# Kernel optimization log

Hardware: AMD Instinct MI355X
Metric: run time of the kernel (lower is better)

The kernel has to match this reference:

```python
import jax, jax.numpy as jnp
import numpy as np

N, E, B = 20000, 160000, 1024
MDIM, EDIM, H, L, PROP = 64, 16, 128, 4, 1000


def _lin(key, fan_in, fan_out, scale=None):
    s = scale if scale is not None else 1.0 / np.sqrt(fan_in)
    return (jax.random.normal(key, (fan_in, fan_out), jnp.float32) * s)


def setup_inputs() -> dict:
    key = jax.random.key(0)
    ks = iter(jax.random.split(key, 64))
    d = {}
    d["x"] = jax.random.normal(next(ks), (N, MDIM), jnp.float32)
    d["pos"] = jax.random.normal(next(ks), (N, 3), jnp.float32)
    d["edge_attr"] = jax.random.normal(next(ks), (E, EDIM), jnp.float32)
    d["edge_index"] = jax.random.randint(next(ks), (2, E), 0, N)
    d["batch"] = jnp.sort(jax.random.randint(next(ks), (N,), 0, B))
    # EGNN embeddings
    d["emb_in_w"] = _lin(next(ks), MDIM, H); d["emb_in_b"] = jnp.zeros((H,), jnp.float32)
    d["emb_out_w"] = _lin(next(ks), H, H); d["emb_out_b"] = jnp.zeros((H,), jnp.float32)
    # per-layer E_GCL params, stacked over layers
    ein = 2 * H + 1 + EDIM  # [h_row, h_col, radial, edge_attr]
    d["edge_w1"] = jnp.stack([_lin(next(ks), ein, H) for _ in range(L)]); d["edge_b1"] = jnp.zeros((L, H), jnp.float32)
    d["edge_w2"] = jnp.stack([_lin(next(ks), H, H) for _ in range(L)]); d["edge_b2"] = jnp.zeros((L, H), jnp.float32)
    d["node_w1"] = jnp.stack([_lin(next(ks), 2 * H, H) for _ in range(L)]); d["node_b1"] = jnp.zeros((L, H), jnp.float32)
    d["node_w2"] = jnp.stack([_lin(next(ks), H, H) for _ in range(L)]); d["node_b2"] = jnp.zeros((L, H), jnp.float32)
    d["coord_w1"] = jnp.stack([_lin(next(ks), H, H) for _ in range(L)]); d["coord_b1"] = jnp.zeros((L, H), jnp.float32)
    d["coord_w2"] = jnp.stack([_lin(next(ks), H, 1, scale=0.001) for _ in range(L)])  # xavier gain=0.001, no bias
    # end_layers: 2 ResBlocks (Dropout->Linear->SiLU->Linear) + head
    d["res_w1"] = jnp.stack([_lin(next(ks), H, H) for _ in range(2)]); d["res_b1"] = jnp.zeros((2, H), jnp.float32)
    d["res_w2"] = jnp.stack([_lin(next(ks), H, H) for _ in range(2)]); d["res_b2"] = jnp.zeros((2, H), jnp.float32)
    d["head_w"] = _lin(next(ks), H, PROP); d["head_b"] = jnp.zeros((PROP,), jnp.float32)
    return d


def _egnn_forward(x, pos, edge_attr, edge_index, batch,
                  emb_in_w, emb_in_b, emb_out_w, emb_out_b,
                  edge_w1, edge_b1, edge_w2, edge_b2,
                  node_w1, node_b1, node_w2, node_b2,
                  coord_w1, coord_b1, coord_w2,
                  res_w1, res_b1, res_w2, res_b2, head_w, head_b):
    silu = jax.nn.silu
    row, col = edge_index[0], edge_index[1]
    h = x @ emb_in_w + emb_in_b                                   # [N, H]
    # edge in-degree counts for coords_agg='mean' (clamped to >=1)
    cnt = jax.ops.segment_sum(jnp.ones((E, 1), h.dtype), row, num_segments=N)
    cnt = jnp.maximum(cnt, 1.0)
    for l in range(L):
        coord_diff = pos[row] - pos[col]                          # [E, 3]
        radial = jnp.sum(coord_diff * coord_diff, axis=-1, keepdims=True)  # [E, 1]
        # edge model
        e_in = jnp.concatenate([h[row], h[col], radial, edge_attr], axis=-1)
        m = silu(silu(e_in @ edge_w1[l] + edge_b1[l]) @ edge_w2[l] + edge_b2[l])  # [E, H]
        # coord model (coords_agg='mean')
        trans = coord_diff * (silu(m @ coord_w1[l] + coord_b1[l]) @ coord_w2[l])  # [E, 3]
        pos = pos + jax.ops.segment_sum(trans, row, num_segments=N) / cnt
        # node model (residual=True)
        agg = jax.ops.segment_sum(m, row, num_segments=N)         # [N, H]
        n_in = jnp.concatenate([h, agg], axis=-1)
        h = h + (silu(n_in @ node_w1[l] + node_b1[l]) @ node_w2[l] + node_b2[l])
    h = h @ emb_out_w + emb_out_b
    g = jax.ops.segment_max(h, batch, num_segments=B)             # [B, H]
    for r in range(2):
        g = g + (silu(g @ res_w1[r] + res_b1[r]) @ res_w2[r] + res_b2[r])
    return g @ head_w + head_b                                    # [B, PROP]


def reference(x, pos, edge_attr, edge_index, batch,
              emb_in_w, emb_in_b, emb_out_w, emb_out_b,
              edge_w1, edge_b1, edge_w2, edge_b2,
              node_w1, node_b1, node_w2, node_b2,
              coord_w1, coord_b1, coord_w2,
              res_w1, res_b1, res_w2, res_b2, head_w, head_b):
    return _egnn_forward(x, pos, edge_attr, edge_index, batch,
                         emb_in_w, emb_in_b, emb_out_w, emb_out_b,
                         edge_w1, edge_b1, edge_w2, edge_b2,
                         node_w1, node_b1, node_w2, node_b2,
                         coord_w1, coord_b1, coord_w2,
                         res_w1, res_b1, res_w2, res_b2, head_w, head_b)
```

## Files before the change

### kernel.cpp

```cpp
#include <hip/hip_runtime.h>
#include <hip/hip_bf16.h>

#define HD 128
#define PROP 1000
#define NPB  8

typedef float f32x4 __attribute__((ext_vector_type(4)));
typedef short s16x8 __attribute__((ext_vector_type(8)));

__device__ __forceinline__ float silu_f(float v) { return v / (1.0f + __expf(-v)); }

__device__ __forceinline__ unsigned short f2bf(float f) {
    union { __hip_bfloat16 h; unsigned short u; } v;
    v.h = __float2bfloat16(f);
    return v.u;
}
__device__ __forceinline__ unsigned pk2(float a, float b) {
    union { __hip_bfloat162 h; unsigned u; } v;
    v.h = __float22bfloat162_rn(make_float2(a, b));
    return v.u;
}
__device__ __forceinline__ float bf2f_lo(unsigned u) { return __uint_as_float(u << 16); }
__device__ __forceinline__ float bf2f_hi(unsigned u) { return __uint_as_float(u & 0xffff0000u); }
__device__ __forceinline__ float4 ld4(const float* p) { return *(const float4*)p; }
__device__ __forceinline__ unsigned enc_max(float f) {
    unsigned u = __float_as_uint(f);
    return (u & 0x80000000u) ? ~u : (u | 0x80000000u);
}


__global__ void counti_kernel(const int* __restrict__ ei, int* __restrict__ cnt, int E) {
    int e = blockIdx.x * 256 + threadIdx.x;
    if (e < E) atomicAdd(&cnt[ei[e]], 1);
}

__global__ __launch_bounds__(1024) void scan_blk(
    const int* __restrict__ cnt, int* __restrict__ excl, int* __restrict__ bsum, int N)
{
    __shared__ int wsum[16], wexc[17];
    const int t = threadIdx.x, lane = t & 63, wid = t >> 6;
    const int gid = blockIdx.x * 1024 + t;
    int v = (gid < N) ? cnt[gid] : 0;
    int incl = v;
    #pragma unroll
    for (int d = 1; d < 64; d <<= 1) {
        int x = __shfl_up(incl, d, 64);
        if (lane >= d) incl += x;
    }
    if (lane == 63) wsum[wid] = incl;
    __syncthreads();
    if (t == 0) {
        int a = 0;
        #pragma unroll
        for (int w2 = 0; w2 < 16; ++w2) { wexc[w2] = a; a += wsum[w2]; }
        wexc[16] = a;
    }
    __syncthreads();
    if (gid < N) excl[gid] = wexc[wid] + incl - v;
    if (t == 0) bsum[blockIdx.x] = wexc[16];
}
__global__ __launch_bounds__(64) void scan_top(int* __restrict__ bsum, int nb) {
    const int lane = threadIdx.x;
    int v = (lane < nb) ? bsum[lane] : 0;
    int incl = v;
    #pragma unroll
    for (int d = 1; d < 64; d <<= 1) {
        int x = __shfl_up(incl, d, 64);
        if (lane >= d) incl += x;
    }
    if (lane < nb) bsum[lane] = incl - v;
}
__global__ void scan_add(const int* __restrict__ excl, const int* __restrict__ bsum,
                         int* __restrict__ rp, int* __restrict__ wp, int N, int E) {
    int gid = blockIdx.x * 256 + threadIdx.x;
    if (gid < N) {
        int r = excl[gid] + bsum[gid >> 10];
        rp[gid] = r; wp[gid] = r;
    }
    if (gid == 0) rp[N] = E;
}

__global__ void scatter_kernel(const int* __restrict__ ei, int* __restrict__ wp,
                               int* __restrict__ perm, int* __restrict__ rows_s,
                               int* __restrict__ cols_s, int E) {
    int e = blockIdx.x * 256 + threadIdx.x;
    if (e < E) {
        int r = ei[e];
        int p = atomicAdd(&wp[r], 1);
        perm[p] = e;
        rows_s[p] = r;
        cols_s[p] = ei[E + e];
    }
}

__global__ void eattr_perm_kernel(const float* __restrict__ eattr, const int* __restrict__ perm,
                                  unsigned short* __restrict__ eperm, int E) {
    int i = blockIdx.x * 256 + threadIdx.x;
    if (i >= E) return;
    const float* src = eattr + (size_t)perm[i] * 16;
    float4 a = ld4(src), b = ld4(src + 4), c = ld4(src + 8), d = ld4(src + 12);
    unsigned short* dst = eperm + (size_t)i * 16;
    *(uint4*)dst       = make_uint4(pk2(a.x, a.y), pk2(a.z, a.w), pk2(b.x, b.y), pk2(b.z, b.w));
    *(uint4*)(dst + 8) = make_uint4(pk2(c.x, c.y), pk2(c.z, c.w), pk2(d.x, d.y), pk2(d.z, d.w));
}

__global__ void prep_all(
    const float* __restrict__ ew1, const float* __restrict__ ew2, const float* __restrict__ cw1,
    const float* __restrict__ nw1, const float* __restrict__ nw2,
    const float* __restrict__ emb_in_w, const float* __restrict__ emb_out_w,
    unsigned short* __restrict__ w1nc, unsigned short* __restrict__ wattr,
    unsigned short* __restrict__ wt2, unsigned short* __restrict__ cwt1,
    unsigned short* __restrict__ nw1t, unsigned short* __restrict__ nw2t,
    unsigned short* __restrict__ wembt, unsigned short* __restrict__ wot,
    unsigned* __restrict__ g_enc, int ng)
{
    int idx = blockIdx.x * 256 + threadIdx.x;
    if (idx < 131072) {
        int k = idx & 127, o2 = (idx >> 7) & 255, l = idx >> 15;
        w1nc[idx] = f2bf(ew1[((size_t)l * 273 + k + ((o2 >> 7) << 7)) * 128 + (o2 & 127)]);
        return;
    }
    idx -= 131072;
    if (idx < 16384) {
        int k = idx & 31, o = (idx >> 5) & 127, l = idx >> 12;
        int ksrc = (k < 16) ? (257 + k) : (k == 16 ? 256 : -1);
        float v = (ksrc >= 0) ? ew1[((size_t)l * 273 + ksrc) * 128 + o] : 0.0f;
        wattr[idx] = f2bf(v);
        return;
    }
    idx -= 16384;
    if (idx < 65536) {
        int k = idx & 127, o = (idx >> 7) & 127, l = idx >> 14;
        int ks = ((k >> 2) & 7) * 16 + ((k >> 5) << 2) + (k & 3);
        wt2[idx] = f2bf(ew2[((size_t)l * 128 + ks) * 128 + o]);
        return;
    }
    idx -= 65536;
    if (idx < 65536) {
        int k = idx & 127, o = (idx >> 7) & 127, l = idx >> 14;
        cwt1[idx] = f2bf(cw1[((size_t)l * 128 + k) * 128 + o]);
        return;
    }
    idx -= 65536;
    if (idx < 131072) {
        int k = idx % 256, o = (idx / 256) & 127, l = idx / (256 * 128);
        nw1t[idx] = f2bf(nw1[((size_t)l * 256 + k) * 128 + o]);
        return;
    }
    idx -= 131072;
    if (idx < 65536) {
        int k = idx & 127, o = (idx >> 7) & 127, l = idx >> 14;
        nw2t[idx] = f2bf(nw2[((size_t)l * 128 + k) * 128 + o]);
        return;
    }
    idx -= 65536;
    if (idx < 8192) {
        int k = idx & 63, o = idx >> 6;
        wembt[idx] = f2bf(emb_in_w[(size_t)k * 128 + o]);
        return;
    }
    idx -= 8192;
    if (idx < 16384) {
        int k = idx & 127, o = idx >> 7;
        wot[idx] = f2bf(emb_out_w[(size_t)k * 128 + o]);
        return;
    }
    idx -= 16384;
    if (idx < ng) g_enc[idx] = 0x007FFFFFu;
}

__global__ __launch_bounds__(128) void emb_pre_kernel(
    const float* __restrict__ x, const unsigned short* __restrict__ wembt,
    const float* __restrict__ bemb,
    const unsigned short* __restrict__ w1nc, const float* __restrict__ b1,
    float* __restrict__ h, unsigned short* __restrict__ apre, int N)
{
    __shared__ __align__(16) char s_xt[32 * 128];
    __shared__ __align__(16) char s_h[32 * 256];
    const int tid = threadIdx.x;
    const int lane = tid & 63, wid = tid >> 6;
    const int lr = lane & 15, kg = lane >> 4;
    const int n0 = blockIdx.x * 32 + wid * 16;
    {
        int n16 = lane >> 2, q = lane & 3;
        int nn = min(n0 + n16, N - 1);
        int sw2 = (n16 & 7) << 4;
        char* row = s_xt + (wid * 16 + n16) * 128;
        #pragma unroll
        for (int it = 0; it < 4; ++it) {
            float4 v = ld4(x + (size_t)nn * 64 + q * 16 + it * 4);
            *(uint2*)(row + ((q * 32 + it * 8) ^ sw2)) = make_uint2(pk2(v.x, v.y), pk2(v.z, v.w));
        }
    }
    const int nd = n0 + lr;
    const int sw = (lr & 7) << 4;
    f32x4 acc[8];
    #pragma unroll
    for (int mf = 0; mf < 8; ++mf) acc[mf] = (f32x4){0.f, 0.f, 0.f, 0.f};
    {
        const char* brow = s_xt + (wid * 16 + lr) * 128;
        for (int ks = 0; ks < 2; ++ks) {
            s16x8 b = *(const s16x8*)(brow + ((ks * 64 + kg * 16) ^ sw));
            #pragma unroll
            for (int mf = 0; mf < 8; ++mf) {
                s16x8 a = *(const s16x8*)(wembt + (size_t)(mf * 16 + lr) * 64 + ks * 32 + kg * 8);
                acc[mf] = __builtin_amdgcn_mfma_f32_16x16x32_bf16(a, b, acc[mf], 0, 0, 0);
            }
        }
    }
    char* hrow = s_h + (wid * 16 + lr) * 256;
    #pragma unroll
    for (int mf = 0; mf < 8; ++mf) {
        f32x4 bb = *(const f32x4*)(bemb + mf * 16 + kg * 4);
        float v0 = acc[mf][0] + bb[0];
        float v1 = acc[mf][1] + bb[1];
        float v2 = acc[mf][2] + bb[2];
        float v3 = acc[mf][3] + bb[3];
        if (nd < N) *(f32x4*)(h + (size_t)nd * HD + mf * 16 + kg * 4) = (f32x4){v0, v1, v2, v3};
        *(uint2*)(hrow + ((mf * 32 + kg * 8) ^ sw)) = make_uint2(pk2(v0, v1), pk2(v2, v3));
    }
    f32x4 acc2[16];
    #pragma unroll
    for (int mf = 0; mf < 16; ++mf) acc2[mf] = (f32x4){0.f, 0.f, 0.f, 0.f};
    for (int ks = 0; ks < 4; ++ks) {
        s16x8 b = *(const s16x8*)(hrow + ((ks * 64 + kg * 16) ^ sw));
        #pragma unroll
        for (int mf = 0; mf < 16; ++mf) {
            s16x8 a = *(const s16x8*)(w1nc + (size_t)(mf * 16 + lr) * 128 + ks * 32 + kg * 8);
            acc2[mf] = __builtin_amdgcn_mfma_f32_16x16x32_bf16(a, b, acc2[mf], 0, 0, 0);
        }
    }
    if (nd < N) {
        #pragma unroll
        for (int mf = 0; mf < 16; ++mf) {
            float b0 = 0.f, b1v = 0.f, b2v = 0.f, b3v = 0.f;
            if (mf < 8) {
                f32x4 bb = *(const f32x4*)(b1 + mf * 16 + kg * 4);
                b0 = bb[0]; b1v = bb[1]; b2v = bb[2]; b3v = bb[3];
            }
            int pos = ((mf >> 3) << 7) + kg * 32 + (mf & 7) * 4;
            *(uint2*)(apre + (size_t)nd * 256 + pos) =
                make_uint2(pk2(acc2[mf][0] + b0, acc2[mf][1] + b1v), pk2(acc2[mf][2] + b2v, acc2[mf][3] + b3v));
        }
    }
}

__global__ __launch_bounds__(64) void edge_compute_kernel(
    const float* __restrict__ pos, const unsigned short* __restrict__ apre,
    const unsigned short* __restrict__ eperm,
    const int* __restrict__ rows_s, const int* __restrict__ cols_s,
    const unsigned short* __restrict__ wattr,
    const unsigned short* __restrict__ wt2, const float* __restrict__ b2,
    const unsigned short* __restrict__ cwt1, const float* __restrict__ cb1,
    const float* __restrict__ cw2,
    unsigned short* __restrict__ medge, float* __restrict__ trans, int E)
{
    __shared__ __align__(16) char s_m[2][16 * 256];
    __shared__ __align__(16) char s_g[2][16 * 256];

    int wg = blockIdx.x;
    {
        int nper = gridDim.x >> 3;
        if ((gridDim.x & 7) == 0) wg = (wg & 7) * nper + (wg >> 3);
    }
    const int lane = threadIdx.x;
    const int lr = lane & 15, kg = lane >> 4;
    const int i0 = wg * 32;
    const int iA = i0 + lr, iB = i0 + 16 + lr;
    const bool vA = iA < E, vB = iB < E;
    const int icA = min(iA, E - 1), icB = min(iB, E - 1);
    const int rA = rows_s[icA], cA = cols_s[icA];
    const int rB = rows_s[icB], cB = cols_s[icB];

    {
        int e = lane >> 2, q = lane & 3;
        int sw2 = (e & 7) << 4;
        #pragma unroll
        for (int t = 0; t < 2; ++t) {
            int ce = cols_s[min(i0 + t * 16 + e, E - 1)];
            const char* src = (const char*)(apre + (size_t)ce * 256 + 128);
            char* dst = s_g[t] + e * 256;
            #pragma unroll
            for (int it = 0; it < 4; ++it) {
                uint4 v = *(const uint4*)(src + it * 64 + q * 16);
                *(uint4*)(dst + ((it * 64 + q * 16) ^ sw2)) = v;
            }
        }
    }

    float dxA = pos[rA*3+0] - pos[cA*3+0];
    float dyA = pos[rA*3+1] - pos[cA*3+1];
    float dzA = pos[rA*3+2] - pos[cA*3+2];
    float dxB = pos[rB*3+0] - pos[cB*3+0];
    float dyB = pos[rB*3+1] - pos[cB*3+1];
    float dzB = pos[rB*3+2] - pos[cB*3+2];
    float radA = dxA*dxA + dyA*dyA + dzA*dzA;
    float radB = dxB*dxB + dyB*dyB + dzB*dzB;

    union { s16x8 v; unsigned u[4]; } battrA, battrB;
    if (kg < 2) {
        battrA.v = *(const s16x8*)(eperm + (size_t)icA * 16 + kg * 8);
        battrB.v = *(const s16x8*)(eperm + (size_t)icB * 16 + kg * 8);
    } else {
        battrA.u[0] = (kg == 2) ? pk2(radA, 0.f) : 0u;
        battrA.u[1] = 0u; battrA.u[2] = 0u; battrA.u[3] = 0u;
        battrB.u[0] = (kg == 2) ? pk2(radB, 0.f) : 0u;
        battrB.u[1] = 0u; battrB.u[2] = 0u; battrB.u[3] = 0u;
    }

    char* mrowA = s_m[0] + lr * 256;
    char* mrowB = s_m[1] + lr * 256;
    const int sw = (lr & 7) << 4;

    f32x4 aA[8], aB[8];
    #pragma unroll
    for (int mf = 0; mf < 8; ++mf) { aA[mf] = (f32x4){0,0,0,0}; aB[mf] = (f32x4){0,0,0,0}; }

    #pragma unroll
    for (int mf = 0; mf < 8; ++mf) {
        s16x8 a = *(const s16x8*)(wattr + (size_t)(mf * 16 + lr) * 32 + kg * 8);
        aA[mf] = __builtin_amdgcn_mfma_f32_16x16x32_bf16(a, battrA.v, aA[mf], 0, 0, 0);
        aB[mf] = __builtin_amdgcn_mfma_f32_16x16x32_bf16(a, battrB.v, aB[mf], 0, 0, 0);
    }
    #pragma unroll
    for (int t = 0; t < 2; ++t) {
        const int r = t ? rB : rA;
        f32x4* acc = t ? aB : aA;
        char* mrow = t ? mrowB : mrowA;
        uint4 rgq[4], cgq[4];
        {
            const unsigned short* rb = apre + (size_t)r * 256 + kg * 32;
            const char* g = s_g[t] + lr * 256;
            #pragma unroll
            for (int q = 0; q < 4; ++q) {
                rgq[q] = *(const uint4*)(rb + q * 8);
                cgq[q] = *(const uint4*)(g + ((kg * 64 + q * 16) ^ sw));
            }
        }
        #pragma unroll
        for (int mf = 0; mf < 8; ++mf) {
            unsigned rlo = ((const unsigned*)&rgq[mf >> 1])[(mf & 1) * 2];
            unsigned rhi = ((const unsigned*)&rgq[mf >> 1])[(mf & 1) * 2 + 1];
            unsigned clo = ((const unsigned*)&cgq[mf >> 1])[(mf & 1) * 2];
            unsigned chi = ((const unsigned*)&cgq[mf >> 1])[(mf & 1) * 2 + 1];
            float v0 = silu_f(acc[mf][0] + bf2f_lo(rlo) + bf2f_lo(clo));
            float v1 = silu_f(acc[mf][1] + bf2f_hi(rlo) + bf2f_hi(clo));
            float v2 = silu_f(acc[mf][2] + bf2f_lo(rhi) + bf2f_lo(chi));
            float v3 = silu_f(acc[mf][3] + bf2f_hi(rhi) + bf2f_hi(chi));
            *(uint2*)(mrow + ((kg * 64 + mf * 8) ^ sw)) = make_uint2(pk2(v0, v1), pk2(v2, v3));
        }
    }

    #pragma unroll
    for (int mf = 0; mf < 8; ++mf) { aA[mf] = (f32x4){0,0,0,0}; aB[mf] = (f32x4){0,0,0,0}; }
    for (int ks = 0; ks < 4; ++ks) {
        s16x8 bA = *(const s16x8*)(mrowA + ((ks * 64 + kg * 16) ^ sw));
        s16x8 bB = *(const s16x8*)(mrowB + ((ks * 64 + kg * 16) ^ sw));
        #pragma unroll
        for (int mf = 0; mf < 8; ++mf) {
            s16x8 a = *(const s16x8*)(wt2 + (size_t)(mf * 16 + lr) * 128 + ks * 32 + kg * 8);
            aA[mf] = __builtin_amdgcn_mfma_f32_16x16x32_bf16(a, bA, aA[mf], 0, 0, 0);
            aB[mf] = __builtin_amdgcn_mfma_f32_16x16x32_bf16(a, bB, aB[mf], 0, 0, 0);
        }
    }
    #pragma unroll
    for (int t = 0; t < 2; ++t) {
        f32x4* acc = t ? aB : aA;
        char* mrow = t ? mrowB : mrowA;
        #pragma unroll
        for (int mf = 0; mf < 8; ++mf) {
            f32x4 bb = *(const f32x4*)(b2 + mf * 16 + kg * 4);
            float v0 = silu_f(acc[mf][0] + bb[0]);
            float v1 = silu_f(acc[mf][1] + bb[1]);
            float v2 = silu_f(acc[mf][2] + bb[2]);
            float v3 = silu_f(acc[mf][3] + bb[3]);
            *(uint2*)(mrow + ((mf * 32 + kg * 8) ^ sw)) = make_uint2(pk2(v0, v1), pk2(v2, v3));
        }
    }

    #pragma unroll
    for (int mf = 0; mf < 8; ++mf) { aA[mf] = (f32x4){0,0,0,0}; aB[mf] = (f32x4){0,0,0,0}; }
    for (int ks = 0; ks < 4; ++ks) {
        s16x8 bA = *(const s16x8*)(mrowA + ((ks * 64 + kg * 16) ^ sw));
        s16x8 bB = *(const s16x8*)(mrowB + ((ks * 64 + kg * 16) ^ sw));
        #pragma unroll
        for (int mf = 0; mf < 8; ++mf) {
            s16x8 a = *(const s16x8*)(cwt1 + (size_t)(mf * 16 + lr) * 128 + ks * 32 + kg * 8);
            aA[mf] = __builtin_amdgcn_mfma_f32_16x16x32_bf16(a, bA, aA[mf], 0, 0, 0);
            aB[mf] = __builtin_amdgcn_mfma_f32_16x16x32_bf16(a, bB, aB[mf], 0, 0, 0);
        }
    }

    {
        int e = lane >> 2, q = lane & 3;
        int sw2 = (e & 7) << 4;
        #pragma unroll
        for (int t = 0; t < 2; ++t) {
            int ie = i0 + t * 16 + e;
            if (ie < E) {
                const char* src = s_m[t] + e * 256;
                char* dst = (char*)(medge + (size_t)ie * HD);
                #pragma unroll
                for (int it = 0; it < 4; ++it) {
                    uint4 v = *(const uint4*)(src + ((it * 64 + q * 16) ^ sw2));
                    *(uint4*)(dst + it * 64 + q * 16) = v;
                }
            }
        }
    }

    #pragma unroll
    for (int t = 0; t < 2; ++t) {
        f32x4* acc = t ? aB : aA;
        float part = 0.f;
        #pragma unroll
        for (int mf = 0; mf < 8; ++mf) {
            f32x4 bb = *(const f32x4*)(cb1 + mf * 16 + kg * 4);
            f32x4 cw = *(const f32x4*)(cw2 + mf * 16 + kg * 4);
            part += silu_f(acc[mf][0] + bb[0]) * cw[0];
            part += silu_f(acc[mf][1] + bb[1]) * cw[1];
            part += silu_f(acc[mf][2] + bb[2]) * cw[2];
            part += silu_f(acc[mf][3] + bb[3]) * cw[3];
        }
        part += __shfl_xor(part, 16, 64);
        part += __shfl_xor(part, 32, 64);
        if (kg == 0) {
            int ie = i0 + t * 16 + lr;
            if (ie < E) {
                float dx = t ? dxB : dxA, dy = t ? dyB : dyA, dz = t ? dzB : dzA;
                *(float4*)(trans + (size_t)ie * 4) = make_float4(dx * part, dy * part, dz * part, 0.f);
            }
        }
    }
}

__global__ __launch_bounds__(64) void node_fused_kernel(
    float* __restrict__ h, const unsigned short* __restrict__ medge,
    const float* __restrict__ trans, const int* __restrict__ rp,
    float* __restrict__ pos,
    const unsigned short* __restrict__ nw1t, const float* __restrict__ nb1,
    const unsigned short* __restrict__ nw2t, const float* __restrict__ nb2,
    const unsigned short* __restrict__ w1nc_next, const float* __restrict__ b1_next,
    unsigned short* __restrict__ apre, int N, int has_next)
{
    __shared__ __align__(16) char s_x[16 * 512];
    const int lane = threadIdx.x;
    const int lr = lane & 15, kg = lane >> 4;
    const int n0 = blockIdx.x * 16;
    {
        int n16 = lane >> 2, q = lane & 3;
        int nn = min(n0 + n16, N - 1);
        int sw2 = (n16 & 7) << 4;
        char* row = s_x + n16 * 512;
        #pragma unroll
        for (int it = 0; it < 8; ++it) {
            int c2 = q * 32 + it * 4;
            float4 v = ld4(h + (size_t)nn * HD + c2);
            *(uint2*)(row + ((c2 * 2) ^ sw2)) = make_uint2(pk2(v.x, v.y), pk2(v.z, v.w));
        }
        const int s = rp[nn], e2 = rp[nn + 1];
        float a[32];
        #pragma unroll
        for (int t = 0; t < 32; ++t) a[t] = 0.f;
        for (int j = s; j < e2; ++j) {
            const unsigned short* mp = medge + (size_t)j * HD + q * 32;
            #pragma unroll
            for (int v4 = 0; v4 < 4; ++v4) {
                uint4 w = *(const uint4*)(mp + v4 * 8);
                a[v4*8+0] += bf2f_lo(w.x); a[v4*8+1] += bf2f_hi(w.x);
                a[v4*8+2] += bf2f_lo(w.y); a[v4*8+3] += bf2f_hi(w.y);
                a[v4*8+4] += bf2f_lo(w.z); a[v4*8+5] += bf2f_hi(w.z);
                a[v4*8+6] += bf2f_lo(w.w); a[v4*8+7] += bf2f_hi(w.w);
            }
        }
        #pragma unroll
        for (int it2 = 0; it2 < 4; ++it2) {
            uint4 w = make_uint4(pk2(a[it2*8+0], a[it2*8+1]), pk2(a[it2*8+2], a[it2*8+3]),
                                 pk2(a[it2*8+4], a[it2*8+5]), pk2(a[it2*8+6], a[it2*8+7]));
            *(uint4*)(row + ((256 + q * 64 + it2 * 16) ^ sw2)) = w;
        }
        if (q < 3 && n0 + n16 < N) {
            float pa = 0.f;
            for (int j = s; j < e2; ++j) pa += trans[(size_t)j * 4 + q];
            pos[(size_t)(n0 + n16) * 3 + q] += pa / fmaxf((float)(e2 - s), 1.0f);
        }
    }
    const int nd = n0 + lr;
    char* brow = s_x + lr * 512;
    const int sw = (lr & 7) << 4;
    f32x4 acc[8];
    #pragma unroll
    for (int mf = 0; mf < 8; ++mf) acc[mf] = (f32x4){0.f, 0.f, 0.f, 0.f};
    for (int ks = 0; ks < 8; ++ks) {
        s16x8 b = *(const s16x8*)(brow + ((ks * 64 + kg * 16) ^ sw));
        #pragma unroll
        for (int mf = 0; mf < 8; ++mf) {
            s16x8 a = *(const s16x8*)(nw1t + (size_t)(mf * 16 + lr) * 256 + ks * 32 + kg * 8);
            acc[mf] = __builtin_amdgcn_mfma_f32_16x16x32_bf16(a, b, acc[mf], 0, 0, 0);
        }
    }
    #pragma unroll
    for (int mf = 0; mf < 8; ++mf) {
        f32x4 bb = *(const f32x4*)(nb1 + mf * 16 + kg * 4);
        float v0 = silu_f(acc[mf][0] + bb[0]);
        float v1 = silu_f(acc[mf][1] + bb[1]);
        float v2 = silu_f(acc[mf][2] + bb[2]);
        float v3 = silu_f(acc[mf][3] + bb[3]);
        *(uint2*)(brow + ((mf * 32 + kg * 8) ^ sw)) = make_uint2(pk2(v0, v1), pk2(v2, v3));
    }
    #pragma unroll
    for (int mf = 0; mf < 8; ++mf) acc[mf] = (f32x4){0.f, 0.f, 0.f, 0.f};
    for (int ks = 0; ks < 4; ++ks) {
        s16x8 b = *(const s16x8*)(brow + ((ks * 64 + kg * 16) ^ sw));
        #pragma unroll
        for (int mf = 0; mf < 8; ++mf) {
            s16x8 a = *(const s16x8*)(nw2t + (size_t)(mf * 16 + lr) * 128 + ks * 32 + kg * 8);
            acc[mf] = __builtin_amdgcn_mfma_f32_16x16x32_bf16(a, b, acc[mf], 0, 0, 0);
        }
    }
    uint2 hpk[8];
    if (nd < N) {
        #pragma unroll
        for (int mf = 0; mf < 8; ++mf) {
            f32x4 bb = *(const f32x4*)(nb2 + mf * 16 + kg * 4);
            float* hp = h + (size_t)nd * HD + mf * 16 + kg * 4;
            f32x4 hv = *(const f32x4*)hp;
            hv[0] += acc[mf][0] + bb[0];
            hv[1] += acc[mf][1] + bb[1];
            hv[2] += acc[mf][2] + bb[2];
            hv[3] += acc[mf][3] + bb[3];
            *(f32x4*)hp = hv;
            hpk[mf] = make_uint2(pk2(hv[0], hv[1]), pk2(hv[2], hv[3]));
        }
    }
    if (!has_next) return;
    #pragma unroll
    for (int mf = 0; mf < 8; ++mf)
        *(uint2*)(brow + ((mf * 32 + kg * 8) ^ sw)) = hpk[mf];
    f32x4 acc2[16];
    #pragma unroll
    for (int mf = 0; mf < 16; ++mf) acc2[mf] = (f32x4){0.f, 0.f, 0.f, 0.f};
    for (int ks = 0; ks < 4; ++ks) {
        s16x8 b = *(const s16x8*)(brow + ((ks * 64 + kg * 16) ^ sw));
        #pragma unroll
        for (int mf = 0; mf < 16; ++mf) {
            s16x8 a = *(const s16x8*)(w1nc_next + (size_t)(mf * 16 + lr) * 128 + ks * 32 + kg * 8);
            acc2[mf] = __builtin_amdgcn_mfma_f32_16x16x32_bf16(a, b, acc2[mf], 0, 0, 0);
        }
    }
    if (nd < N) {
        #pragma unroll
        for (int mf = 0; mf < 16; ++mf) {
            float b0 = 0.f, b1v = 0.f, b2v = 0.f, b3v = 0.f;
            if (mf < 8) {
                f32x4 bb = *(const f32x4*)(b1_next + mf * 16 + kg * 4);
                b0 = bb[0]; b1v = bb[1]; b2v = bb[2]; b3v = bb[3];
            }
            int pos2 = ((mf >> 3) << 7) + kg * 32 + (mf & 7) * 4;
            *(uint2*)(apre + (size_t)nd * 256 + pos2) =
                make_uint2(pk2(acc2[mf][0] + b0, acc2[mf][1] + b1v), pk2(acc2[mf][2] + b2v, acc2[mf][3] + b3v));
        }
    }
}

__global__ __launch_bounds__(64) void embout_mfma_kernel(
    const float* __restrict__ h, const unsigned short* __restrict__ wot,
    const float* __restrict__ b, const int* __restrict__ batch,
    unsigned* __restrict__ g_enc, int N)
{
    __shared__ __align__(16) char s_h[16 * 256];
    __shared__ __align__(16) float s_out[16 * 128];
    const int lane = threadIdx.x;
    const int lr = lane & 15, kg = lane >> 4;
    const int n0 = blockIdx.x * 16;
    {
        int n16 = lane >> 2, q = lane & 3;
        int nn = min(n0 + n16, N - 1);
        int sw2 = (n16 & 7) << 4;
        char* row = s_h + n16 * 256;
        #pragma unroll
        for (int it = 0; it < 8; ++it) {
            int c2 = q * 32 + it * 4;
            float4 v = ld4(h + (size_t)nn * HD + c2);
            *(uint2*)(row + ((c2 * 2) ^ sw2)) = make_uint2(pk2(v.x, v.y), pk2(v.z, v.w));
        }
    }
    const char* brow = s_h + lr * 256;
    const int sw = (lr & 7) << 4;
    f32x4 acc[8];
    #pragma unroll
    for (int mf = 0; mf < 8; ++mf) acc[mf] = (f32x4){0.f, 0.f, 0.f, 0.f};
    for (int ks = 0; ks < 4; ++ks) {
        s16x8 bv = *(const s16x8*)(brow + ((ks * 64 + kg * 16) ^ sw));
        #pragma unroll
        for (int mf = 0; mf < 8; ++mf) {
            s16x8 a = *(const s16x8*)(wot + (size_t)(mf * 16 + lr) * 128 + ks * 32 + kg * 8);
            acc[mf] = __builtin_amdgcn_mfma_f32_16x16x32_bf16(a, bv, acc[mf], 0, 0, 0);
        }
    }
    #pragma unroll
    for (int mf = 0; mf < 8; ++mf) {
        f32x4 bb = *(const f32x4*)(b + mf * 16 + kg * 4);
        f32x4 v = { acc[mf][0] + bb[0], acc[mf][1] + bb[1], acc[mf][2] + bb[2], acc[mf][3] + bb[3] };
        *(f32x4*)(s_out + lr * 128 + mf * 16 + kg * 4) = v;
    }
    const int nmax = min(16, N - n0);
    float m0 = -3.4e38f, m1 = -3.4e38f;
    int cur = batch[n0];
    for (int e = 0; e < nmax; ++e) {
        int bi = batch[n0 + e];
        if (bi != cur) {
            atomicMax(&g_enc[(size_t)cur * HD + lane], enc_max(m0));
            atomicMax(&g_enc[(size_t)cur * HD + 64 + lane], enc_max(m1));
            m0 = -3.4e38f; m1 = -3.4e38f; cur = bi;
        }
        m0 = fmaxf(m0, s_out[e * 128 + lane]);
        m1 = fmaxf(m1, s_out[e * 128 + 64 + lane]);
    }
    atomicMax(&g_enc[(size_t)cur * HD + lane], enc_max(m0));
    atomicMax(&g_enc[(size_t)cur * HD + 64 + lane], enc_max(m1));
}

__global__ __launch_bounds__(128) void resblock_kernel(
    const unsigned* __restrict__ g_enc,
    const float* __restrict__ rw1, const float* __restrict__ rb1,
    const float* __restrict__ rw2, const float* __restrict__ rb2,
    float* __restrict__ g)
{
    __shared__ float s_g[HD];
    __shared__ float s_t[HD];
    const int b = blockIdx.x, j = threadIdx.x;
    unsigned u = g_enc[(size_t)b * HD + j];
    float v = (u & 0x80000000u) ? __uint_as_float(u & 0x7FFFFFFFu) : __uint_as_float(~u);
    s_g[j] = v;
    __syncthreads();
    for (int r = 0; r < 2; ++r) {
        float a1 = rb1[r * HD + j];
        for (int k = 0; k < HD; ++k) a1 += s_g[k] * rw1[(size_t)r * HD * HD + (size_t)k * HD + j];
        s_t[j] = silu_f(a1);
        __syncthreads();
        float a2 = rb2[r * HD + j];
        for (int k = 0; k < HD; ++k) a2 += s_t[k] * rw2[(size_t)r * HD * HD + (size_t)k * HD + j];
        __syncthreads();
        s_g[j] += a2;
        __syncthreads();
    }
    g[(size_t)b * HD + j] = s_g[j];
}

__global__ __launch_bounds__(256) void head_kernel(
    const float* __restrict__ g, const float* __restrict__ hw, const float* __restrict__ hb,
    float* __restrict__ out, int B)
{
    __shared__ __align__(16) float s_g[HD][8];
    const int b0 = blockIdx.y * 8;
    const int p = blockIdx.x * 256 + threadIdx.x;
    for (int t = threadIdx.x; t < 8 * HD; t += 256) {
        int b = t & 7, k = t >> 3;
        s_g[k][b] = g[(size_t)min(b0 + b, B - 1) * HD + k];
    }
    __syncthreads();
    if (p >= PROP) return;
    float hbp = hb[p];
    float acc[8];
    #pragma unroll
    for (int b = 0; b < 8; ++b) acc[b] = hbp;
    for (int k = 0; k < HD; ++k) {
        float w = hw[(size_t)k * PROP + p];
        float4 g0 = *(const float4*)&s_g[k][0];
        float4 g1 = *(const float4*)&s_g[k][4];
        acc[0] += g0.x * w; acc[1] += g0.y * w; acc[2] += g0.z * w; acc[3] += g0.w * w;
        acc[4] += g1.x * w; acc[5] += g1.y * w; acc[6] += g1.z * w; acc[7] += g1.w * w;
    }
    #pragma unroll
    for (int b = 0; b < 8; ++b)
        if (b0 + b < B) out[(size_t)(b0 + b) * PROP + p] = acc[b];
}

extern "C" void kernel_launch(void* const* d_in, const int* in_sizes, int n_in,
                              void* d_out, int out_size, void* d_ws, size_t ws_size,
                              hipStream_t stream)
{
    const float* x        = (const float*)d_in[0];
    const float* pos_in   = (const float*)d_in[1];
    const float* eattr    = (const float*)d_in[2];
    const int*   ei       = (const int*)d_in[3];
    const int*   batch    = (const int*)d_in[4];
    const float* emb_in_w = (const float*)d_in[5];
    const float* emb_in_b = (const float*)d_in[6];
    const float* emb_out_w= (const float*)d_in[7];
    const float* emb_out_b= (const float*)d_in[8];
    const float* ew1 = (const float*)d_in[9];
    const float* eb1 = (const float*)d_in[10];
    const float* ew2 = (const float*)d_in[11];
    const float* eb2 = (const float*)d_in[12];
    const float* nw1 = (const float*)d_in[13];
    const float* nb1 = (const float*)d_in[14];
    const float* nw2 = (const float*)d_in[15];
    const float* nb2 = (const float*)d_in[16];
    const float* cw1 = (const float*)d_in[17];
    const float* cb1 = (const float*)d_in[18];
    const float* cw2 = (const float*)d_in[19];
    const float* rw1 = (const float*)d_in[20];
    const float* rb1 = (const float*)d_in[21];
    const float* rw2 = (const float*)d_in[22];
    const float* rb2 = (const float*)d_in[23];
    const float* hw  = (const float*)d_in[24];
    const float* hb  = (const float*)d_in[25];
    float* out = (float*)d_out;
    (void)ws_size;

    const int N = in_sizes[0] / 64;
    const int E = in_sizes[2] / 16;
    const int B = out_size / PROP;

    float* wsf = (float*)d_ws;
    float* pos_cur = wsf;   wsf += (size_t)N * 3;
    float* h       = wsf;   wsf += (size_t)N * HD;
    float* g       = wsf;   wsf += (size_t)B * HD;
    float* trans   = wsf;   wsf += (size_t)E * 4;
    wsf += (4 - (((size_t)(wsf - (float*)d_ws)) & 3)) & 3;
    unsigned short* apre  = (unsigned short*)wsf;
    unsigned short* eperm = apre  + (size_t)N * 256;
    unsigned short* w1nc  = eperm + (size_t)E * 16;
    unsigned short* wattr = w1nc  + (size_t)4 * 256 * 128;
    unsigned short* wt2   = wattr + (size_t)4 * 128 * 32;
    unsigned short* cwt1  = wt2   + (size_t)4 * 128 * 128;
    unsigned short* nw1t  = cwt1  + (size_t)4 * 128 * 128;
    unsigned short* nw2t  = nw1t  + (size_t)4 * 128 * 256;
    unsigned short* wembt = nw2t  + (size_t)4 * 128 * 128;
    unsigned short* wot   = wembt + (size_t)128 * 64;
    unsigned short* medge = wot   + (size_t)128 * 128;
    int* ip   = (int*)(medge + (size_t)E * HD);
    unsigned* g_enc = (unsigned*)ip;  ip += (size_t)B * HD;
    int* cnt_i = ip;  ip += N;
    int* rp    = ip;  ip += N + 1;
    int* wp    = ip;  ip += N;
    int* excl  = ip;  ip += N;
    int* bsum  = ip;  ip += 64;
    int* perm  = ip;  ip += E;
    int* rows_s= ip;  ip += E;
    int* cols_s= ip;  ip += E;

    const int ng = B * HD;
    const int prep_total = 131072 + 16384 + 65536 + 65536 + 131072 + 65536 + 8192 + 16384 + ng;
    prep_all<<<(prep_total + 255) / 256, 256, 0, stream>>>(
        ew1, ew2, cw1, nw1, nw2, emb_in_w, emb_out_w,
        w1nc, wattr, wt2, cwt1, nw1t, nw2t, wembt, wot, g_enc, ng);

    hipMemsetAsync(cnt_i, 0, (size_t)N * sizeof(int), stream);
    counti_kernel<<<(E + 255) / 256, 256, 0, stream>>>(ei, cnt_i, E);
    const int nb = (N + 1023) / 1024;
    scan_blk<<<nb, 1024, 0, stream>>>(cnt_i, excl, bsum, N);
    scan_top<<<1, 64, 0, stream>>>(bsum, nb);
    scan_add<<<(N + 255) / 256, 256, 0, stream>>>(excl, bsum, rp, wp, N, E);
    scatter_kernel<<<(E + 255) / 256, 256, 0, stream>>>(ei, wp, perm, rows_s, cols_s, E);
    eattr_perm_kernel<<<(E + 255) / 256, 256, 0, stream>>>(eattr, perm, eperm, E);

    hipMemcpyAsync(pos_cur, pos_in, (size_t)N * 3 * sizeof(float),
                   hipMemcpyDeviceToDevice, stream);

    emb_pre_kernel<<<(N + 31) / 32, 128, 0, stream>>>(x, wembt, emb_in_b, w1nc, eb1, h, apre, N);
    const int nblk = (N + 15) / 16;
    for (int l = 0; l < 4; ++l) {
        edge_compute_kernel<<<(E + 31) / 32, 64, 0, stream>>>(
            pos_cur, apre, eperm, rows_s, cols_s,
            wattr + (size_t)l * 128 * 32,
            wt2  + (size_t)l * 128 * 128, eb2 + (size_t)l * HD,
            cwt1 + (size_t)l * 128 * 128, cb1 + (size_t)l * HD,
            cw2 + (size_t)l * HD,
            medge, trans, E);
        node_fused_kernel<<<nblk, 64, 0, stream>>>(
            h, medge, trans, rp, pos_cur,
            nw1t + (size_t)l * 128 * 256, nb1 + (size_t)l * HD,
            nw2t + (size_t)l * 128 * 128, nb2 + (size_t)l * HD,
            w1nc + (size_t)(l + 1 < 4 ? l + 1 : 0) * 256 * 128,
            eb1 + (size_t)(l + 1 < 4 ? l + 1 : 0) * HD,
            apre, N, l < 3 ? 1 : 0);
    }

    embout_mfma_kernel<<<nblk, 64, 0, stream>>>(h, wot, emb_out_b, batch, g_enc, N);
    resblock_kernel<<<B, 128, 0, stream>>>(g_enc, rw1, rb1, rw2, rb2, g);
    head_kernel<<<dim3((PROP + 255) / 256, (B + 7) / 8), 256, 0, stream>>>(g, hw, hb, out, B);
}
```

Measured before the change: 604.0 us.

## Process two node tiles per block and read column features directly in edge kernel

```diff
diff --git a/kernel.cpp b/kernel.cpp
--- a/kernel.cpp
+++ b/kernel.cpp
@@ -3,7 +3,6 @@
 
 #define HD 128
 #define PROP 1000
-#define NPB  8
 
 typedef float f32x4 __attribute__((ext_vector_type(4)));
 typedef short s16x8 __attribute__((ext_vector_type(8)));
@@ -256,7 +255,6 @@
     unsigned short* __restrict__ medge, float* __restrict__ trans, int E)
 {
     __shared__ __align__(16) char s_m[2][16 * 256];
-    __shared__ __align__(16) char s_g[2][16 * 256];
 
     int wg = blockIdx.x;
     {
@@ -267,26 +265,9 @@
     const int lr = lane & 15, kg = lane >> 4;
     const int i0 = wg * 32;
     const int iA = i0 + lr, iB = i0 + 16 + lr;
-    const bool vA = iA < E, vB = iB < E;
     const int icA = min(iA, E - 1), icB = min(iB, E - 1);
     const int rA = rows_s[icA], cA = cols_s[icA];
     const int rB = rows_s[icB], cB = cols_s[icB];
-
-    {
-        int e = lane >> 2, q = lane & 3;
-        int sw2 = (e & 7) << 4;
-        #pragma unroll
-        for (int t = 0; t < 2; ++t) {
-            int ce = cols_s[min(i0 + t * 16 + e, E - 1)];
-            const char* src = (const char*)(apre + (size_t)ce * 256 + 128);
-            char* dst = s_g[t] + e * 256;
-            #pragma unroll
-            for (int it = 0; it < 4; ++it) {
-                uint4 v = *(const uint4*)(src + it * 64 + q * 16);
-                *(uint4*)(dst + ((it * 64 + q * 16) ^ sw2)) = v;
-            }
-        }
-    }
 
     float dxA = pos[rA*3+0] - pos[cA*3+0];
     float dyA = pos[rA*3+1] - pos[cA*3+1];
@@ -325,16 +306,17 @@
     #pragma unroll
     for (int t = 0; t < 2; ++t) {
         const int r = t ? rB : rA;
+        const int c = t ? cB : cA;
         f32x4* acc = t ? aB : aA;
         char* mrow = t ? mrowB : mrowA;
         uint4 rgq[4], cgq[4];
         {
             const unsigned short* rb = apre + (size_t)r * 256 + kg * 32;
-            const char* g = s_g[t] + lr * 256;
+            const unsigned short* cb = apre + (size_t)c * 256 + 128 + kg * 32;
             #pragma unroll
             for (int q = 0; q < 4; ++q) {
                 rgq[q] = *(const uint4*)(rb + q * 8);
-                cgq[q] = *(const uint4*)(g + ((kg * 64 + q * 16) ^ sw));
+                cgq[q] = *(const uint4*)(cb + q * 8);
             }
         }
         #pragma unroll
@@ -443,15 +425,17 @@
     const unsigned short* __restrict__ w1nc_next, const float* __restrict__ b1_next,
     unsigned short* __restrict__ apre, int N, int has_next)
 {
-    __shared__ __align__(16) char s_x[16 * 512];
+    __shared__ __align__(16) char s_x[2][16 * 512];
     const int lane = threadIdx.x;
     const int lr = lane & 15, kg = lane >> 4;
-    const int n0 = blockIdx.x * 16;
-    {
+    const int n0 = blockIdx.x * 32;
+    #pragma unroll
+    for (int t = 0; t < 2; ++t) {
         int n16 = lane >> 2, q = lane & 3;
-        int nn = min(n0 + n16, N - 1);
+        int nid = n0 + t * 16 + n16;
+        int nn = min(nid, N - 1);
         int sw2 = (n16 & 7) << 4;
-        char* row = s_x + n16 * 512;
+        char* row = s_x[t] + n16 * 512;
         #pragma unroll
         for (int it = 0; it < 8; ++it) {
             int c2 = q * 32 + it * 4;
@@ -461,7 +445,7 @@
         const int s = rp[nn], e2 = rp[nn + 1];
         float a[32];
         #pragma unroll
-        for (int t = 0; t < 32; ++t) a[t] = 0.f;
+        for (int u = 0; u < 32; ++u) a[u] = 0.f;
         for (int j = s; j < e2; ++j) {
             const unsigned short* mp = medge + (size_t)j * HD + q * 32;
             #pragma unroll
@@ -479,86 +463,105 @@
                                  pk2(a[it2*8+4], a[it2*8+5]), pk2(a[it2*8+6], a[it2*8+7]));
             *(uint4*)(row + ((256 + q * 64 + it2 * 16) ^ sw2)) = w;
         }
-        if (q < 3 && n0 + n16 < N) {
+        if (q < 3 && nid < N) {
             float pa = 0.f;
             for (int j = s; j < e2; ++j) pa += trans[(size_t)j * 4 + q];
-            pos[(size_t)(n0 + n16) * 3 + q] += pa / fmaxf((float)(e2 - s), 1.0f);
-        }
-    }
-    const int nd = n0 + lr;
-    char* brow = s_x + lr * 512;
+            pos[(size_t)nid * 3 + q] += pa / fmaxf((float)(e2 - s), 1.0f);
+        }
+    }
+    const int ndA = n0 + lr, ndB = n0 + 16 + lr;
+    char* browA = s_x[0] + lr * 512;
+    char* browB = s_x[1] + lr * 512;
     const int sw = (lr & 7) << 4;
-    f32x4 acc[8];
-    #pragma unroll
-    for (int mf = 0; mf < 8; ++mf) acc[mf] = (f32x4){0.f, 0.f, 0.f, 0.f};
+
+    f32x4 aA[8], aB[8];
+    #pragma unroll
+    for (int mf = 0; mf < 8; ++mf) { aA[mf] = (f32x4){0,0,0,0}; aB[mf] = (f32x4){0,0,0,0}; }
     for (int ks = 0; ks < 8; ++ks) {
-        s16x8 b = *(const s16x8*)(brow + ((ks * 64 + kg * 16) ^ sw));
+        s16x8 bA = *(const s16x8*)(browA + ((ks * 64 + kg * 16) ^ sw));
+        s16x8 bB = *(const s16x8*)(browB + ((ks * 64 + kg * 16) ^ sw));
         #pragma unroll
         for (int mf = 0; mf < 8; ++mf) {
             s16x8 a = *(const s16x8*)(nw1t + (size_t)(mf * 16 + lr) * 256 + ks * 32 + kg * 8);
-            acc[mf] = __builtin_amdgcn_mfma_f32_16x16x32_bf16(a, b, acc[mf], 0, 0, 0);
-        }
-    }
-    #pragma unroll
-    for (int mf = 0; mf < 8; ++mf) {
-        f32x4 bb = *(const f32x4*)(nb1 + mf * 16 + kg * 4);
-        float v0 = silu_f(acc[mf][0] + bb[0]);
-        float v1 = silu_f(acc[mf][1] + bb[1]);
-        float v2 = silu_f(acc[mf][2] + bb[2]);
-        float v3 = silu_f(acc[mf][3] + bb[3]);
-        *(uint2*)(brow + ((mf * 32 + kg * 8) ^ sw)) = make_uint2(pk2(v0, v1), pk2(v2, v3));
-    }
-    #pragma unroll
-    for (int mf = 0; mf < 8; ++mf) acc[mf] = (f32x4){0.f, 0.f, 0.f, 0.f};
+            aA[mf] = __builtin_amdgcn_mfma_f32_16x16x32_bf16(a, bA, aA[mf], 0, 0, 0);
+            aB[mf] = __builtin_amdgcn_mfma_f32_16x16x32_bf16(a, bB, aB[mf], 0, 0, 0);
+        }
+    }
+    #pragma unroll
+    for (int t = 0; t < 2; ++t) {
+        f32x4* acc = t ? aB : aA;
+        char* brow = t ? browB : browA;
+        #pragma unroll
+        for (int mf = 0; mf < 8; ++mf) {
+            f32x4 bb = *(const f32x4*)(nb1 + mf * 16 + kg * 4);
+            float v0 = silu_f(acc[mf][0] + bb[0]);
+            float v1 = silu_f(acc[mf][1] + bb[1]);
+            float v2 = silu_f(acc[mf][2] + bb[2]);
+            float v3 = silu_f(acc[mf][3] + bb[3]);
+            *(uint2*)(brow + ((mf * 32 + kg * 8) ^ sw)) = make_uint2(pk2(v0, v1), pk2(v2, v3));
+        }
+    }
+    #pragma unroll
+    for (int mf = 0; mf < 8; ++mf) { aA[mf] = (f32x4){0,0,0,0}; aB[mf] = (f32x4){0,0,0,0}; }
     for (int ks = 0; ks < 4; ++ks) {
-        s16x8 b = *(const s16x8*)(brow + ((ks * 64 + kg * 16) ^ sw));
+        s16x8 bA = *(const s16x8*)(browA + ((ks * 64 + kg * 16) ^ sw));
+        s16x8 bB = *(const s16x8*)(browB + ((ks * 64 + kg * 16) ^ sw));
         #pragma unroll
         for (int mf = 0; mf < 8; ++mf) {
             s16x8 a = *(const s16x8*)(nw2t + (size_t)(mf * 16 + lr) * 128 + ks * 32 + kg * 8);
-            acc[mf] = __builtin_amdgcn_mfma_f32_16x16x32_bf16(a, b, acc[mf], 0, 0, 0);
-        }
-    }
-    uint2 hpk[8];
-    if (nd < N) {
-        #pragma unroll
-        for (int mf = 0; mf < 8; ++mf) {
-            f32x4 bb = *(const f32x4*)(nb2 + mf * 16 + kg * 4);
-            float* hp = h + (size_t)nd * HD + mf * 16 + kg * 4;
-            f32x4 hv = *(const f32x4*)hp;
-            hv[0] += acc[mf][0] + bb[0];
-            hv[1] += acc[mf][1] + bb[1];
-            hv[2] += acc[mf][2] + bb[2];
-            hv[3] += acc[mf][3] + bb[3];
-            *(f32x4*)hp = hv;
-            hpk[mf] = make_uint2(pk2(hv[0], hv[1]), pk2(hv[2], hv[3]));
+            aA[mf] = __builtin_amdgcn_mfma_f32_16x16x32_bf16(a, bA, aA[mf], 0, 0, 0);
+            aB[mf] = __builtin_amdgcn_mfma_f32_16x16x32_bf16(a, bB, aB[mf], 0, 0, 0);
+        }
+    }
+    #pragma unroll
+    for (int t = 0; t < 2; ++t) {
+        const int nd = t ? ndB : ndA;
+        f32x4* acc = t ? aB : aA;
+        char* brow = t ? browB : browA;
+        if (nd < N) {
+            #pragma unroll
+            for (int mf = 0; mf < 8; ++mf) {
+                f32x4 bb = *(const f32x4*)(nb2 + mf * 16 + kg * 4);
+                float* hp = h + (size_t)nd * HD + mf * 16 + kg * 4;
+                f32x4 hv = *(const f32x4*)hp;
+                hv[0] += acc[mf][0] + bb[0];
+                hv[1] += acc[mf][1] + bb[1];
+                hv[2] += acc[mf][2] + bb[2];
+                hv[3] += acc[mf][3] + bb[3];
+                *(f32x4*)hp = hv;
+                *(uint2*)(brow + ((mf * 32 + kg * 8) ^ sw)) =
+                    make_uint2(pk2(hv[0], hv[1]), pk2(hv[2], hv[3]));
+            }
         }
     }
     if (!has_next) return;
     #pragma unroll
-    for (int mf = 0; mf < 8; ++mf)
-        *(uint2*)(brow + ((mf * 32 + kg * 8) ^ sw)) = hpk[mf];
-    f32x4 acc2[16];
-    #pragma unroll
-    for (int mf = 0; mf < 16; ++mf) acc2[mf] = (f32x4){0.f, 0.f, 0.f, 0.f};
-    for (int ks = 0; ks < 4; ++ks) {
-        s16x8 b = *(const s16x8*)(brow + ((ks * 64 + kg * 16) ^ sw));
-        #pragma unroll
-        for (int mf = 0; mf < 16; ++mf) {
-            s16x8 a = *(const s16x8*)(w1nc_next + (size_t)(mf * 16 + lr) * 128 + ks * 32 + kg * 8);
-            acc2[mf] = __builtin_amdgcn_mfma_f32_16x16x32_bf16(a, b, acc2[mf], 0, 0, 0);
-        }
-    }
-    if (nd < N) {
-        #pragma unroll
-        for (int mf = 0; mf < 16; ++mf) {
-            float b0 = 0.f, b1v = 0.f, b2v = 0.f, b3v = 0.f;
-            if (mf < 8) {
-                f32x4 bb = *(const f32x4*)(b1_next + mf * 16 + kg * 4);
-                b0 = bb[0]; b1v = bb[1]; b2v = bb[2]; b3v = bb[3];
-            }
-            int pos2 = ((mf >> 3) << 7) + kg * 32 + (mf & 7) * 4;
-            *(uint2*)(apre + (size_t)nd * 256 + pos2) =
-                make_uint2(pk2(acc2[mf][0] + b0, acc2[mf][1] + b1v), pk2(acc2[mf][2] + b2v, acc2[mf][3] + b3v));
+    for (int t = 0; t < 2; ++t) {
+        const int nd = t ? ndB : ndA;
+        const char* brow = t ? browB : browA;
+        f32x4 acc2[16];
+        #pragma unroll
+        for (int mf = 0; mf < 16; ++mf) acc2[mf] = (f32x4){0.f, 0.f, 0.f, 0.f};
+        for (int ks = 0; ks < 4; ++ks) {
+            s16x8 b = *(const s16x8*)(brow + ((ks * 64 + kg * 16) ^ sw));
+            #pragma unroll
+            for (int mf = 0; mf < 16; ++mf) {
+                s16x8 a = *(const s16x8*)(w1nc_next + (size_t)(mf * 16 + lr) * 128 + ks * 32 + kg * 8);
+                acc2[mf] = __builtin_amdgcn_mfma_f32_16x16x32_bf16(a, b, acc2[mf], 0, 0, 0);
+            }
+        }
+        if (nd < N) {
+            #pragma unroll
+            for (int mf = 0; mf < 16; ++mf) {
+                float b0 = 0.f, b1v = 0.f, b2v = 0.f, b3v = 0.f;
+                if (mf < 8) {
+                    f32x4 bb = *(const f32x4*)(b1_next + mf * 16 + kg * 4);
+                    b0 = bb[0]; b1v = bb[1]; b2v = bb[2]; b3v = bb[3];
+                }
+                int pos2 = ((mf >> 3) << 7) + kg * 32 + (mf & 7) * 4;
+                *(uint2*)(apre + (size_t)nd * 256 + pos2) =
+                    make_uint2(pk2(acc2[mf][0] + b0, acc2[mf][1] + b1v), pk2(acc2[mf][2] + b2v, acc2[mf][3] + b3v));
+            }
         }
     }
 }
@@ -761,7 +764,7 @@
                    hipMemcpyDeviceToDevice, stream);
 
     emb_pre_kernel<<<(N + 31) / 32, 128, 0, stream>>>(x, wembt, emb_in_b, w1nc, eb1, h, apre, N);
-    const int nblk = (N + 15) / 16;
+    const int nblk32 = (N + 31) / 32;
     for (int l = 0; l < 4; ++l) {
         edge_compute_kernel<<<(E + 31) / 32, 64, 0, stream>>>(
             pos_cur, apre, eperm, rows_s, cols_s,
@@ -770,7 +773,7 @@
             cwt1 + (size_t)l * 128 * 128, cb1 + (size_t)l * HD,
             cw2 + (size_t)l * HD,
             medge, trans, E);
-        node_fused_kernel<<<nblk, 64, 0, stream>>>(
+        node_fused_kernel<<<nblk32, 64, 0, stream>>>(
             h, medge, trans, rp, pos_cur,
             nw1t + (size_t)l * 128 * 256, nb1 + (size_t)l * HD,
             nw2t + (size_t)l * 128 * 128, nb2 + (size_t)l * HD,
@@ -779,7 +782,7 @@
             apre, N, l < 3 ? 1 : 0);
     }
 
-    embout_mfma_kernel<<<nblk, 64, 0, stream>>>(h, wot, emb_out_b, batch, g_enc, N);
+    embout_mfma_kernel<<<(N + 15) / 16, 64, 0, stream>>>(h, wot, emb_out_b, batch, g_enc, N);
     resblock_kernel<<<B, 128, 0, stream>>>(g_enc, rw1, rb1, rw2, rb2, g);
     head_kernel<<<dim3((PROP + 255) / 256, (B + 7) / 8), 256, 0, stream>>>(g, hw, hb, out, B);
 }
```

Result: faster. 551.5 us, median of 2 (-8.7%).
